# Kernel optimization log

Measured on AMD Instinct MI355X. Metric: run time of the kernel, lower is better.

The kernel has to match this reference:

```python
import jax, jax.numpy as jnp
import numpy as np

B, S, H, R = 64, 2048, 512, 256
NEG = -1.0e9


def setup_inputs() -> dict:
    key = jax.random.key(0)
    ks = jax.random.split(key, 12)
    sc_h = 1.0 / np.sqrt(H)
    sc_r = 1.0 / np.sqrt(R)
    return {
        "sent_h": jax.random.normal(ks[0], (B, S, H), jnp.float32),
        "rel": jax.random.normal(ks[1], (B, R), jnp.float32),
        "pool": jax.random.normal(ks[2], (B, H), jnp.float32),
        "mask": jax.random.randint(ks[3], (B, S), 0, 2, jnp.int32),
        "Wg_w": jax.random.normal(ks[4], (H, H), jnp.float32) * sc_h,
        "Wg_b": jnp.zeros((H,), jnp.float32),
        "Wh_w": jax.random.normal(ks[5], (H, H), jnp.float32) * sc_h,
        "Wh_b": jnp.zeros((H,), jnp.float32),
        "Wr_w": jax.random.normal(ks[6], (H, R), jnp.float32) * sc_r,
        "Wr_b": jnp.zeros((H,), jnp.float32),
        "alpha_w": jax.random.normal(ks[7], (1, H), jnp.float32) * sc_h,
        "alpha_b": jnp.zeros((1,), jnp.float32),
    }


def reference(sent_h, rel, pool, mask, Wg_w, Wg_b, Wh_w, Wh_b, Wr_w, Wr_b, alpha_w, alpha_b):
    # linear projections (torch Linear: x @ W.T + b)
    relation = rel @ Wr_w.T + Wr_b          # [B, H]
    sent = jnp.einsum('bsh,kh->bsk', sent_h, Wh_w) + Wh_b  # [B, S, H]
    global_sen = pool @ Wg_w.T + Wg_b       # [B, H]
    mix = jnp.tanh(relation[:, None, :] + sent + global_sen[:, None, :])  # [B, S, H]
    weight = jnp.einsum('bsh,h->bs', mix, alpha_w[0]) + alpha_b[0]        # [B, S]
    weight = jnp.where(mask == 0, NEG, weight)
    weight_ = jax.nn.softmax(weight, axis=-1)
    att_res = jnp.einsum('bs,bsh->bh', weight_, sent)  # [B, H]
    return (att_res, weight_)
```

## Files before the change

### kernel.cpp

```cpp
#include <hip/hip_runtime.h>
#include <cstdint>
#include <cstddef>

#define B_ 64
#define S_ 2048
#define H_ 512
#define R_ 256
#define M_ (B_ * S_)
#define NEGV (-1.0e9f)

typedef short short8 __attribute__((ext_vector_type(8)));
typedef unsigned short u16x8 __attribute__((ext_vector_type(8)));
typedef float f32x4 __attribute__((ext_vector_type(4)));
typedef unsigned short u16;

__device__ __forceinline__ u16 f2b(float x) {
    union { float f; uint32_t u; } c; c.f = x;
    uint32_t u = c.u;
    uint32_t r = (u + 0x7fffu + ((u >> 16) & 1u)) >> 16;
    return (u16)r;
}
__device__ __forceinline__ float b2f(u16 u) {
    union { uint32_t u; float f; } c; c.u = ((uint32_t)u) << 16;
    return c.f;
}
__device__ __forceinline__ uint32_t pk2(float lo, float hi) {
    uint32_t r;
    asm("v_cvt_pk_bf16_f32 %0, %1, %2" : "=v"(r) : "v"(lo), "v"(hi));
    return r;
}
__device__ __forceinline__ void load_lds16(const void* g, void* l) {
    __builtin_amdgcn_global_load_lds((__attribute__((address_space(1))) void*)g,
                                     (__attribute__((address_space(3))) void*)l,
                                     16, 0, 0);
}

__global__ void k_base(const float* __restrict__ rel, const float* __restrict__ pool,
                       const float* __restrict__ Wg_w, const float* __restrict__ Wg_b,
                       const float* __restrict__ Wh_b,
                       const float* __restrict__ Wr_w, const float* __restrict__ Wr_b,
                       const float* __restrict__ whw, float* __restrict__ base,
                       u16* __restrict__ whwb) {
    int tid = threadIdx.x;
    {
        int gi = blockIdx.x * 256 + tid;
        float4 v = ((const float4*)whw)[gi];
        ushort4 o; o.x = f2b(v.x); o.y = f2b(v.y); o.z = f2b(v.z); o.w = f2b(v.w);
        ((ushort4*)whwb)[gi] = o;
    }
    int b = blockIdx.x >> 2, q = blockIdx.x & 3;
    __shared__ __attribute__((aligned(16))) float srel[R_];
    __shared__ __attribute__((aligned(16))) float spool[H_];
    __shared__ float accs[128];
    srel[tid & 255] = rel[b * R_ + (tid & 255)];
    for (int i = tid; i < H_; i += 256) spool[i] = pool[b * H_ + i];
    __syncthreads();
    int kk = tid & 127, half = tid >> 7;
    int k = q * 128 + kk;
    float acc = 0.f;
    if (half == 0) {
        acc = Wr_b[k] + Wg_b[k] + Wh_b[k];
        const float4* wr = (const float4*)(Wr_w + (size_t)k * R_);
        #pragma unroll 8
        for (int r4 = 0; r4 < R_ / 4; ++r4) {
            float4 w = wr[r4]; float4 x = ((const float4*)srel)[r4];
            acc += w.x * x.x + w.y * x.y + w.z * x.z + w.w * x.w;
        }
        const float4* wg = (const float4*)(Wg_w + (size_t)k * H_);
        #pragma unroll 8
        for (int h4 = 0; h4 < 32; ++h4) {
            float4 w = wg[h4]; float4 x = ((const float4*)spool)[h4];
            acc += w.x * x.x + w.y * x.y + w.z * x.z + w.w * x.w;
        }
    } else {
        const float4* wg = (const float4*)(Wg_w + (size_t)k * H_);
        #pragma unroll 8
        for (int h4 = 32; h4 < 128; ++h4) {
            float4 w = wg[h4]; float4 x = ((const float4*)spool)[h4];
            acc += w.x * x.x + w.y * x.y + w.z * x.z + w.w * x.w;
        }
    }
    if (half) accs[kk] = acc;
    __syncthreads();
    if (!half) base[b * H_ + k] = acc + accs[kk];
}

__launch_bounds__(256)
__global__ void k_gemm(const float* __restrict__ A32,
                       const u16* __restrict__ Bw,
                       const float* __restrict__ base,
                       const float* __restrict__ alpha,
                       float* __restrict__ partial)
{
    const int K = 512;
    int j = blockIdx.x;
    int xcd  = j & 7;
    int slot = j >> 3;
    int nb   = slot & 3;
    int mb   = (slot >> 2) * 8 + xcd;
    int m0 = mb * 128;
    int n0 = nb * 128;
    int b  = m0 >> 11;

    int tid = threadIdx.x;
    int w  = tid >> 6;
    int l  = tid & 63;
    int wm = w & 1, wn = w >> 1;
    int lr = l & 15;
    int lq = l >> 4;

    __shared__ __attribute__((aligned(16))) u16 smA[2][128 * 64];
    __shared__ __attribute__((aligned(16))) u16 smB[2][128 * 64];
    __shared__ float red[2][2][64];

    f32x4 zero = {0.f, 0.f, 0.f, 0.f};
    f32x4 acc[4][4];
    #pragma unroll
    for (int i = 0; i < 4; ++i)
        #pragma unroll
        for (int jj = 0; jj < 4; ++jj) acc[i][jj] = zero;

    int arow[4], acolg[4];
    #pragma unroll
    for (int i = 0; i < 4; ++i) {
        int c = w * 4 + i;
        arow[i]  = (c >> 1) * 16 + lr;
        acolg[i] = (c & 1) * 32 + lq * 8;
    }

    float4 av[4][2];

    auto LOAD_A = [&](int kt) {
        int k0 = kt * 64;
        #pragma unroll
        for (int i = 0; i < 4; ++i) {
            const float4* ga = (const float4*)(A32 + (size_t)(m0 + arow[i]) * K + k0 + acolg[i]);
            av[i][0] = ga[0];
            av[i][1] = ga[1];
        }
    };
    auto WRITE_A = [&](int buf) {
        #pragma unroll
        for (int i = 0; i < 4; ++i) {
            uint4 pv;
            pv.x = pk2(av[i][0].x, av[i][0].y);
            pv.y = pk2(av[i][0].z, av[i][0].w);
            pv.z = pk2(av[i][1].x, av[i][1].y);
            pv.w = pk2(av[i][1].z, av[i][1].w);
            *(uint4*)(smA[buf] + (w * 4 + i) * 512 + l * 8) = pv;
        }
    };
    auto STAGE_B = [&](int buf, int kt) {
        int k0 = kt * 64;
        #pragma unroll
        for (int i = 0; i < 4; ++i) {
            int c  = w * 4 + i;
            int mf = c >> 1, kc = c & 1;
            int row = mf * 16 + lr;
            int col = k0 + kc * 32 + lq * 8;
            const u16* gb = Bw + (size_t)(n0 + row) * K + col;
            load_lds16(gb, smB[buf] + c * 512);
        }
    };

    LOAD_A(0);
    STAGE_B(0, 0);
    WRITE_A(0);
    __syncthreads();

    #pragma unroll
    for (int kt = 0; kt < 8; ++kt) {
        int cur = kt & 1;
        if (kt < 7) {
            LOAD_A(kt + 1);
            STAGE_B(cur ^ 1, kt + 1);
        }
        __builtin_amdgcn_s_setprio(1);
        #pragma unroll
        for (int kc = 0; kc < 2; ++kc) {
            short8 af[4], bf[4];
            #pragma unroll
            for (int mi = 0; mi < 4; ++mi)
                af[mi] = *(const short8*)(smA[cur] + ((wm * 4 + mi) * 2 + kc) * 512 + l * 8);
            #pragma unroll
            for (int ni = 0; ni < 4; ++ni)
                bf[ni] = *(const short8*)(smB[cur] + ((wn * 4 + ni) * 2 + kc) * 512 + l * 8);
            #pragma unroll
            for (int mi = 0; mi < 4; ++mi)
                #pragma unroll
                for (int ni = 0; ni < 4; ++ni)
                    acc[mi][ni] = __builtin_amdgcn_mfma_f32_16x16x32_bf16(af[mi], bf[ni], acc[mi][ni], 0, 0, 0);
        }
        __builtin_amdgcn_s_setprio(0);
        if (kt < 7) WRITE_A(cur ^ 1);
        __syncthreads();
    }

    const float C2 = 2.8853900817779268f;
    float base2[4], a2[4];
    float asum = 0.f;
    #pragma unroll
    for (int ni = 0; ni < 4; ++ni) {
        int n = n0 + wn * 64 + ni * 16 + lr;
        base2[ni] = C2 * base[b * H_ + n];
        float al  = alpha[n];
        a2[ni] = 2.0f * al;
        asum  += al;
    }
    #pragma unroll
    for (int mi = 0; mi < 4; ++mi) {
        #pragma unroll
        for (int r = 0; r < 4; ++r) {
            float s = asum;
            #pragma unroll
            for (int ni = 0; ni < 4; ++ni) {
                float f  = fmaf(acc[mi][ni][r], C2, base2[ni]);
                float e  = __builtin_amdgcn_exp2f(f);
                float rr = __builtin_amdgcn_rcpf(e + 1.0f);
                s = fmaf(-a2[ni], rr, s);
            }
            s += __shfl_xor(s, 1);
            s += __shfl_xor(s, 2);
            s += __shfl_xor(s, 4);
            s += __shfl_xor(s, 8);
            if (lr == 0) red[wm][wn][mi * 16 + lq * 4 + r] = s;
        }
    }
    __syncthreads();
    if (tid < 128) {
        int wmi = tid >> 6, row = tid & 63;
        float sum = red[wmi][0][row] + red[wmi][1][row];
        partial[(size_t)nb * M_ + m0 + wmi * 64 + row] = sum;
    }
}

__global__ void k_softmax(const float* __restrict__ partial, const int* __restrict__ mask,
                          const float* __restrict__ alpha_b, float* __restrict__ wout) {
    int b = blockIdx.x;
    int tid = threadIdx.x;
    __shared__ float sred[8];
    float x[8];
    float ab = alpha_b[0];
    float lmax = -3.0e38f;
    #pragma unroll
    for (int jj = 0; jj < 8; ++jj) {
        int s = tid + jj * 256;
        size_t m = (size_t)b * S_ + s;
        float v = partial[m] + partial[(size_t)M_ + m] + partial[2 * (size_t)M_ + m] + partial[3 * (size_t)M_ + m] + ab;
        if (mask[b * S_ + s] == 0) v = NEGV;
        x[jj] = v;
        lmax = fmaxf(lmax, v);
    }
    #pragma unroll
    for (int off = 1; off < 64; off <<= 1) lmax = fmaxf(lmax, __shfl_xor(lmax, off));
    int wv = tid >> 6, l = tid & 63;
    if (l == 0) sred[wv] = lmax;
    __syncthreads();
    float gmax = fmaxf(fmaxf(sred[0], sred[1]), fmaxf(sred[2], sred[3]));
    float lsum = 0.f;
    #pragma unroll
    for (int jj = 0; jj < 8; ++jj) { x[jj] = __expf(x[jj] - gmax); lsum += x[jj]; }
    #pragma unroll
    for (int off = 1; off < 64; off <<= 1) lsum += __shfl_xor(lsum, off);
    if (l == 0) sred[4 + wv] = lsum;
    __syncthreads();
    float inv = 1.f / (sred[4] + sred[5] + sred[6] + sred[7]);
    #pragma unroll
    for (int jj = 0; jj < 8; ++jj) {
        int s = tid + jj * 256;
        wout[(size_t)b * S_ + s] = x[jj] * inv;
    }
}

__global__ void k_wsum(const float* __restrict__ sent, const float* __restrict__ wrow_g,
                       float* __restrict__ tpart) {
    int b  = blockIdx.x >> 4;
    int ss = blockIdx.x & 15;
    int tid = threadIdx.x;
    __shared__ float wrow[128];
    if (tid < 128) wrow[tid] = wrow_g[(size_t)b * S_ + ss * 128 + tid];
    __syncthreads();
    const float* bp = sent + ((size_t)b * S_ + (size_t)ss * 128) * H_ + tid * 2;
    float ax = 0.f, ay = 0.f;
    for (int r0 = 0; r0 < 128; r0 += 8) {
        float2 v[8];
        #pragma unroll
        for (int u = 0; u < 8; ++u)
            v[u] = *(const float2*)(bp + (size_t)(r0 + u) * H_);
        #pragma unroll
        for (int u = 0; u < 8; ++u) {
            float wgt = wrow[r0 + u];
            ax = fmaf(wgt, v[u].x, ax);
            ay = fmaf(wgt, v[u].y, ay);
        }
    }
    float* tp = tpart + ((size_t)ss * B_ + b) * H_ + tid * 2;
    tp[0] = ax; tp[1] = ay;
}

__global__ void k_att(const float* __restrict__ tpart, const float* __restrict__ Whw,
                      const float* __restrict__ Whb, float* __restrict__ out) {
    int tid = threadIdx.x;
    int b = blockIdx.x >> 2, q = blockIdx.x & 3;
    __shared__ __attribute__((aligned(16))) float st[H_];
    __shared__ float accs[128];
    for (int i = tid; i < H_; i += 256) {
        float s = 0.f;
        #pragma unroll
        for (int ss = 0; ss < 16; ++ss)
            s += tpart[((size_t)ss * B_ + b) * H_ + i];
        st[i] = s;
    }
    __syncthreads();
    int hh = tid & 127, half = tid >> 7;
    int h = q * 128 + hh;
    const float4* wr = (const float4*)(Whw + (size_t)h * H_) + half * 64;
    const float4* sx = (const float4*)st + half * 64;
    float acc = 0.f;
    #pragma unroll 8
    for (int i = 0; i < 64; ++i) {
        float4 w = wr[i]; float4 x = sx[i];
        acc += w.x * x.x + w.y * x.y + w.z * x.z + w.w * x.w;
    }
    if (half) accs[hh] = acc;
    __syncthreads();
    if (!half) out[(size_t)b * H_ + h] = acc + accs[hh] + Whb[h];
}

extern "C" void kernel_launch(void* const* d_in, const int* in_sizes, int n_in,
                              void* d_out, int out_size, void* d_ws, size_t ws_size,
                              hipStream_t stream) {
    const float* sent_h  = (const float*)d_in[0];
    const float* rel     = (const float*)d_in[1];
    const float* pool    = (const float*)d_in[2];
    const int*   mask    = (const int*)d_in[3];
    const float* Wg_w    = (const float*)d_in[4];
    const float* Wg_b    = (const float*)d_in[5];
    const float* Wh_w    = (const float*)d_in[6];
    const float* Wh_b    = (const float*)d_in[7];
    const float* Wr_w    = (const float*)d_in[8];
    const float* Wr_b    = (const float*)d_in[9];
    const float* alpha_w = (const float*)d_in[10];
    const float* alpha_b = (const float*)d_in[11];
    float* out = (float*)d_out;

    char* ws = (char*)d_ws;
    u16*   whwb    = (u16*)ws;
    float* base    = (float*)(ws + 524288);
    float* partial = (float*)(ws + 524288 + 131072);
    float* tpart   = (float*)(ws + 524288 + 131072 + 2097152);

    float* att_out = out;
    float* w_out   = out + B_ * H_;

    k_base<<<dim3(256), dim3(256), 0, stream>>>(rel, pool, Wg_w, Wg_b, Wh_b, Wr_w, Wr_b, Wh_w, base, whwb);
    k_gemm<<<dim3((M_ / 128) * 4), dim3(256), 0, stream>>>(sent_h, whwb, base, alpha_w, partial);
    k_softmax<<<dim3(B_), dim3(256), 0, stream>>>(partial, mask, alpha_b, w_out);
    k_wsum<<<dim3(B_ * 16), dim3(256), 0, stream>>>(sent_h, w_out, tpart);
    k_att<<<dim3(256), dim3(256), 0, stream>>>(tpart, Wh_w, Wh_b, att_out);
}
```

Measured before the change: 572.5 us.

## Prefetch A tiles two stages ahead with explicit vmcnt waits in GEMM loop

```diff
diff --git a/kernel.cpp b/kernel.cpp
--- a/kernel.cpp
+++ b/kernel.cpp
@@ -14,6 +14,9 @@
 typedef float f32x4 __attribute__((ext_vector_type(4)));
 typedef unsigned short u16;
 
+#define VMCNT(N)  asm volatile("s_waitcnt vmcnt(" #N ")" ::: "memory")
+#define LGKM0()   asm volatile("s_waitcnt lgkmcnt(0)" ::: "memory")
+
 __device__ __forceinline__ u16 f2b(float x) {
     union { float f; uint32_t u; } c; c.f = x;
     uint32_t u = c.u;
@@ -28,6 +31,11 @@
     uint32_t r;
     asm("v_cvt_pk_bf16_f32 %0, %1, %2" : "=v"(r) : "v"(lo), "v"(hi));
     return r;
+}
+__device__ __forceinline__ float4 gload4(const float4* p) {
+    float4 d;
+    asm volatile("global_load_dwordx4 %0, %1, off" : "=v"(d) : "v"(p));
+    return d;
 }
 __device__ __forceinline__ void load_lds16(const void* g, void* l) {
     __builtin_amdgcn_global_load_lds((__attribute__((address_space(1))) void*)g,
@@ -95,9 +103,9 @@
     const int K = 512;
     int j = blockIdx.x;
     int xcd  = j & 7;
-    int slot = j >> 3;
-    int nb   = slot & 3;
-    int mb   = (slot >> 2) * 8 + xcd;
+    int slot0 = j >> 3;
+    int nb   = slot0 & 3;
+    int mb   = (slot0 >> 2) * 8 + xcd;
     int m0 = mb * 128;
     int n0 = nb * 128;
     int b  = m0 >> 11;
@@ -128,25 +136,25 @@
         acolg[i] = (c & 1) * 32 + lq * 8;
     }
 
-    float4 av[4][2];
-
-    auto LOAD_A = [&](int kt) {
+    float4 av[2][4][2];
+
+    auto LOAD_A = [&](int slot, int kt) {
         int k0 = kt * 64;
         #pragma unroll
         for (int i = 0; i < 4; ++i) {
             const float4* ga = (const float4*)(A32 + (size_t)(m0 + arow[i]) * K + k0 + acolg[i]);
-            av[i][0] = ga[0];
-            av[i][1] = ga[1];
+            av[slot][i][0] = gload4(ga);
+            av[slot][i][1] = gload4(ga + 1);
         }
     };
-    auto WRITE_A = [&](int buf) {
+    auto WRITE_A = [&](int buf, int slot) {
         #pragma unroll
         for (int i = 0; i < 4; ++i) {
             uint4 pv;
-            pv.x = pk2(av[i][0].x, av[i][0].y);
-            pv.y = pk2(av[i][0].z, av[i][0].w);
-            pv.z = pk2(av[i][1].x, av[i][1].y);
-            pv.w = pk2(av[i][1].z, av[i][1].w);
+            pv.x = pk2(av[slot][i][0].x, av[slot][i][0].y);
+            pv.y = pk2(av[slot][i][0].z, av[slot][i][0].w);
+            pv.z = pk2(av[slot][i][1].x, av[slot][i][1].y);
+            pv.w = pk2(av[slot][i][1].z, av[slot][i][1].w);
             *(uint4*)(smA[buf] + (w * 4 + i) * 512 + l * 8) = pv;
         }
     };
@@ -163,18 +171,21 @@
         }
     };
 
-    LOAD_A(0);
+    LOAD_A(0, 0);
     STAGE_B(0, 0);
-    WRITE_A(0);
-    __syncthreads();
+    LOAD_A(1, 1);
+    VMCNT(12); __builtin_amdgcn_sched_barrier(0);
+    WRITE_A(0, 0);
+    VMCNT(8);
+    LGKM0();
+    __builtin_amdgcn_s_barrier();
 
     #pragma unroll
     for (int kt = 0; kt < 8; ++kt) {
-        int cur = kt & 1;
-        if (kt < 7) {
-            LOAD_A(kt + 1);
-            STAGE_B(cur ^ 1, kt + 1);
-        }
+        const int cur = kt & 1, nxt = cur ^ 1;
+        __builtin_amdgcn_sched_barrier(0);
+        if (kt < 7) STAGE_B(nxt, kt + 1);
+        if (kt < 6) LOAD_A(cur, kt + 2);
         __builtin_amdgcn_s_setprio(1);
         #pragma unroll
         for (int kc = 0; kc < 2; ++kc) {
@@ -192,9 +203,16 @@
                     acc[mi][ni] = __builtin_amdgcn_mfma_f32_16x16x32_bf16(af[mi], bf[ni], acc[mi][ni], 0, 0, 0);
         }
         __builtin_amdgcn_s_setprio(0);
-        if (kt < 7) WRITE_A(cur ^ 1);
-        __syncthreads();
-    }
+        if (kt < 7) {
+            if (kt < 6) { VMCNT(12); } else { VMCNT(4); }
+            __builtin_amdgcn_sched_barrier(0);
+            WRITE_A(nxt, (kt + 1) & 1);
+            if (kt < 6) { VMCNT(8); } else { VMCNT(0); }
+        }
+        LGKM0();
+        __builtin_amdgcn_s_barrier();
+    }
+    __builtin_amdgcn_sched_barrier(0);
 
     const float C2 = 2.8853900817779268f;
     float base2[4], a2[4];
```

Measured after the change: 566.8 us. Within noise of the previous version (-1.0%).

## Enlarge GEMM tile to 256x256 with 8 waves and explicit waitcnt pipelining

Applied to the files above, without the earlier changes.

```diff
diff --git a/kernel.cpp b/kernel.cpp
--- a/kernel.cpp
+++ b/kernel.cpp
@@ -14,20 +14,25 @@
 typedef float f32x4 __attribute__((ext_vector_type(4)));
 typedef unsigned short u16;
 
+#define VMCNT(N)  asm volatile("s_waitcnt vmcnt(" #N ")" ::: "memory")
+#define LGKM0()   asm volatile("s_waitcnt lgkmcnt(0)" ::: "memory")
+#define SB0()     __builtin_amdgcn_sched_barrier(0)
+
 __device__ __forceinline__ u16 f2b(float x) {
     union { float f; uint32_t u; } c; c.f = x;
     uint32_t u = c.u;
     uint32_t r = (u + 0x7fffu + ((u >> 16) & 1u)) >> 16;
     return (u16)r;
 }
-__device__ __forceinline__ float b2f(u16 u) {
-    union { uint32_t u; float f; } c; c.u = ((uint32_t)u) << 16;
-    return c.f;
-}
 __device__ __forceinline__ uint32_t pk2(float lo, float hi) {
     uint32_t r;
     asm("v_cvt_pk_bf16_f32 %0, %1, %2" : "=v"(r) : "v"(lo), "v"(hi));
     return r;
+}
+__device__ __forceinline__ float4 gload4(const float4* p) {
+    float4 d;
+    asm volatile("global_load_dwordx4 %0, %1, off" : "=v"(d) : "v"(p));
+    return d;
 }
 __device__ __forceinline__ void load_lds16(const void* g, void* l) {
     __builtin_amdgcn_global_load_lds((__attribute__((address_space(1))) void*)g,
@@ -85,7 +90,7 @@
     if (!half) base[b * H_ + k] = acc + accs[kk];
 }
 
-__launch_bounds__(256)
+__launch_bounds__(512, 1)
 __global__ void k_gemm(const float* __restrict__ A32,
                        const u16* __restrict__ Bw,
                        const float* __restrict__ base,
@@ -94,12 +99,11 @@
 {
     const int K = 512;
     int j = blockIdx.x;
-    int xcd  = j & 7;
-    int slot = j >> 3;
-    int nb   = slot & 3;
-    int mb   = (slot >> 2) * 8 + xcd;
-    int m0 = mb * 128;
-    int n0 = nb * 128;
+    int sid = (j & 7) * 128 + (j >> 3);
+    int nb  = sid & 1;
+    int mbt = sid >> 1;
+    int m0 = mbt * 256;
+    int n0 = nb * 256;
     int b  = m0 >> 11;
 
     int tid = threadIdx.x;
@@ -109,34 +113,28 @@
     int lr = l & 15;
     int lq = l >> 4;
 
-    __shared__ __attribute__((aligned(16))) u16 smA[2][128 * 64];
-    __shared__ __attribute__((aligned(16))) u16 smB[2][128 * 64];
-    __shared__ float red[2][2][64];
+    __shared__ __attribute__((aligned(16))) u16 smA[2][32 * 512];
+    __shared__ __attribute__((aligned(16))) u16 smB[2][32 * 512];
+    __shared__ float red[2][4][128];
 
     f32x4 zero = {0.f, 0.f, 0.f, 0.f};
-    f32x4 acc[4][4];
-    #pragma unroll
-    for (int i = 0; i < 4; ++i)
+    f32x4 acc[8][4];
+    #pragma unroll
+    for (int i = 0; i < 8; ++i)
         #pragma unroll
         for (int jj = 0; jj < 4; ++jj) acc[i][jj] = zero;
 
-    int arow[4], acolg[4];
-    #pragma unroll
-    for (int i = 0; i < 4; ++i) {
-        int c = w * 4 + i;
-        arow[i]  = (c >> 1) * 16 + lr;
-        acolg[i] = (c & 1) * 32 + lq * 8;
-    }
-
     float4 av[4][2];
 
-    auto LOAD_A = [&](int kt) {
-        int k0 = kt * 64;
+    auto LOAD_A = [&](int t) {
+        int k0 = t * 64;
         #pragma unroll
         for (int i = 0; i < 4; ++i) {
-            const float4* ga = (const float4*)(A32 + (size_t)(m0 + arow[i]) * K + k0 + acolg[i]);
-            av[i][0] = ga[0];
-            av[i][1] = ga[1];
+            int c = w * 4 + i;
+            const float4* ga = (const float4*)(A32 + (size_t)(m0 + (c >> 1) * 16 + lr) * K
+                                               + k0 + (c & 1) * 32 + lq * 8);
+            av[i][0] = gload4(ga);
+            av[i][1] = gload4(ga + 1);
         }
     };
     auto WRITE_A = [&](int buf) {
@@ -150,50 +148,61 @@
             *(uint4*)(smA[buf] + (w * 4 + i) * 512 + l * 8) = pv;
         }
     };
-    auto STAGE_B = [&](int buf, int kt) {
-        int k0 = kt * 64;
+    auto STAGE_B = [&](int buf, int t) {
+        int k0 = t * 64;
         #pragma unroll
         for (int i = 0; i < 4; ++i) {
-            int c  = w * 4 + i;
-            int mf = c >> 1, kc = c & 1;
-            int row = mf * 16 + lr;
-            int col = k0 + kc * 32 + lq * 8;
-            const u16* gb = Bw + (size_t)(n0 + row) * K + col;
+            int c = w * 4 + i;
+            const u16* gb = Bw + (size_t)(n0 + (c >> 1) * 16 + lr) * K
+                            + k0 + (c & 1) * 32 + lq * 8;
             load_lds16(gb, smB[buf] + c * 512);
         }
+    };
+    auto PHASE = [&](int cur, int kc, int mh) {
+        short8 af[4], bf[4];
+        #pragma unroll
+        for (int jj = 0; jj < 4; ++jj)
+            af[jj] = *(const short8*)(smA[cur] + ((wm * 8 + mh * 4 + jj) * 2 + kc) * 512 + l * 8);
+        #pragma unroll
+        for (int n = 0; n < 4; ++n)
+            bf[n] = *(const short8*)(smB[cur] + ((wn * 4 + n) * 2 + kc) * 512 + l * 8);
+        __builtin_amdgcn_s_setprio(1);
+        #pragma unroll
+        for (int jj = 0; jj < 4; ++jj)
+            #pragma unroll
+            for (int n = 0; n < 4; ++n)
+                acc[mh * 4 + jj][n] = __builtin_amdgcn_mfma_f32_16x16x32_bf16(af[jj], bf[n], acc[mh * 4 + jj][n], 0, 0, 0);
+        __builtin_amdgcn_s_setprio(0);
     };
 
     LOAD_A(0);
     STAGE_B(0, 0);
+    VMCNT(4); SB0();
     WRITE_A(0);
-    __syncthreads();
-
-    #pragma unroll
-    for (int kt = 0; kt < 8; ++kt) {
-        int cur = kt & 1;
-        if (kt < 7) {
-            LOAD_A(kt + 1);
-            STAGE_B(cur ^ 1, kt + 1);
-        }
-        __builtin_amdgcn_s_setprio(1);
-        #pragma unroll
-        for (int kc = 0; kc < 2; ++kc) {
-            short8 af[4], bf[4];
-            #pragma unroll
-            for (int mi = 0; mi < 4; ++mi)
-                af[mi] = *(const short8*)(smA[cur] + ((wm * 4 + mi) * 2 + kc) * 512 + l * 8);
-            #pragma unroll
-            for (int ni = 0; ni < 4; ++ni)
-                bf[ni] = *(const short8*)(smB[cur] + ((wn * 4 + ni) * 2 + kc) * 512 + l * 8);
-            #pragma unroll
-            for (int mi = 0; mi < 4; ++mi)
-                #pragma unroll
-                for (int ni = 0; ni < 4; ++ni)
-                    acc[mi][ni] = __builtin_amdgcn_mfma_f32_16x16x32_bf16(af[mi], bf[ni], acc[mi][ni], 0, 0, 0);
-        }
-        __builtin_amdgcn_s_setprio(0);
-        if (kt < 7) WRITE_A(cur ^ 1);
-        __syncthreads();
+    VMCNT(0); LGKM0();
+    __builtin_amdgcn_s_barrier();
+    SB0();
+
+    #pragma unroll
+    for (int t = 0; t < 8; ++t) {
+        const int cur = t & 1, nxt = cur ^ 1;
+        if (t < 7) LOAD_A(t + 1);
+        PHASE(cur, 0, 0);
+        __builtin_amdgcn_s_barrier();
+        if (t < 7) STAGE_B(nxt, t + 1);
+        PHASE(cur, 0, 1);
+        __builtin_amdgcn_s_barrier();
+        PHASE(cur, 1, 0);
+        __builtin_amdgcn_s_barrier();
+        PHASE(cur, 1, 1);
+        if (t < 7) {
+            VMCNT(4); SB0();
+            WRITE_A(nxt);
+            VMCNT(0);
+        }
+        LGKM0();
+        __builtin_amdgcn_s_barrier();
+        SB0();
     }
 
     const float C2 = 2.8853900817779268f;
@@ -208,7 +217,7 @@
         asum  += al;
     }
     #pragma unroll
-    for (int mi = 0; mi < 4; ++mi) {
+    for (int mi = 0; mi < 8; ++mi) {
         #pragma unroll
         for (int r = 0; r < 4; ++r) {
             float s = asum;
@@ -227,10 +236,10 @@
         }
     }
     __syncthreads();
-    if (tid < 128) {
-        int wmi = tid >> 6, row = tid & 63;
-        float sum = red[wmi][0][row] + red[wmi][1][row];
-        partial[(size_t)nb * M_ + m0 + wmi * 64 + row] = sum;
+    if (tid < 256) {
+        int wm2 = tid >> 7, row = tid & 127;
+        float sum = red[wm2][0][row] + red[wm2][1][row] + red[wm2][2][row] + red[wm2][3][row];
+        partial[(size_t)nb * M_ + m0 + wm2 * 128 + row] = sum;
     }
 }
 
@@ -246,7 +255,7 @@
     for (int jj = 0; jj < 8; ++jj) {
         int s = tid + jj * 256;
         size_t m = (size_t)b * S_ + s;
-        float v = partial[m] + partial[(size_t)M_ + m] + partial[2 * (size_t)M_ + m] + partial[3 * (size_t)M_ + m] + ab;
+        float v = partial[m] + partial[(size_t)M_ + m] + ab;
         if (mask[b * S_ + s] == 0) v = NEGV;
         x[jj] = v;
         lmax = fmaxf(lmax, v);
@@ -348,13 +357,13 @@
     u16*   whwb    = (u16*)ws;
     float* base    = (float*)(ws + 524288);
     float* partial = (float*)(ws + 524288 + 131072);
-    float* tpart   = (float*)(ws + 524288 + 131072 + 2097152);
+    float* tpart   = (float*)(ws + 524288 + 131072 + 1048576);
 
     float* att_out = out;
     float* w_out   = out + B_ * H_;
 
     k_base<<<dim3(256), dim3(256), 0, stream>>>(rel, pool, Wg_w, Wg_b, Wh_b, Wr_w, Wr_b, Wh_w, base, whwb);
-    k_gemm<<<dim3((M_ / 128) * 4), dim3(256), 0, stream>>>(sent_h, whwb, base, alpha_w, partial);
+    k_gemm<<<dim3(1024), dim3(512), 0, stream>>>(sent_h, whwb, base, alpha_w, partial);
     k_softmax<<<dim3(B_), dim3(256), 0, stream>>>(partial, mask, alpha_b, w_out);
     k_wsum<<<dim3(B_ * 16), dim3(256), 0, stream>>>(sent_h, w_out, tpart);
     k_att<<<dim3(256), dim3(256), 0, stream>>>(tpart, Wh_w, Wh_b, att_out);
```

Result: faster. 524.4 us (-8.4%).
